# Optimization experiments

Hardware: AMD Instinct MI355X
Metric: run time of the kernel (lower is better)

Reference implementation:

```python
import jax, jax.numpy as jnp
import numpy as np

N_NODES = 50000
N_EDGES = 640000
N_GRAPHS = 64
IN_DIM, HID, OUT_DIM = 128, 256, 4


def gcn_conv(x, src, dst, W, b, n_nodes):
    """PyG GCNConv: linear transform, then sym-normalized aggregation with self-loops."""
    h = x @ W  # [N, out]
    deg = jnp.zeros((n_nodes,), h.dtype).at[dst].add(1.0) + 1.0  # +1 self-loop
    dinv = jax.lax.rsqrt(deg)  # deg >= 1 always
    norm = dinv[src] * dinv[dst]  # [E]
    msg = h[src] * norm[:, None]  # [E, out]  gather + scale
    agg = jax.ops.segment_sum(msg, dst, num_segments=n_nodes)  # scatter-add
    agg = agg + h * (dinv * dinv)[:, None]  # self-loop contribution
    return agg + b


def global_mean_pool(x, batch, num_graphs):
    s = jax.ops.segment_sum(x, batch, num_segments=num_graphs)
    cnt = jax.ops.segment_sum(jnp.ones((x.shape[0],), x.dtype), batch, num_segments=num_graphs)
    return s / jnp.clip(cnt, 1.0)[:, None]


def setup_inputs() -> dict:
    key = jax.random.key(0)
    ks = jax.random.split(key, 8)
    x = jax.random.normal(ks[0], (N_NODES, IN_DIM), jnp.float32)
    src = jax.random.randint(ks[1], (N_EDGES,), 0, N_NODES, jnp.int64 if jax.config.jax_enable_x64 else jnp.int32)
    dst = jax.random.randint(ks[2], (N_EDGES,), 0, N_NODES, src.dtype)
    batch = jnp.sort(jax.random.randint(ks[3], (N_NODES,), 0, N_GRAPHS, src.dtype))
    W1 = jax.random.normal(ks[4], (IN_DIM, HID), jnp.float32) * (1.0 / np.sqrt(IN_DIM))
    b1 = jnp.zeros((HID,), jnp.float32)
    W2 = jax.random.normal(ks[5], (HID, HID // 2), jnp.float32) * (1.0 / np.sqrt(HID))
    b2 = jnp.zeros((HID // 2,), jnp.float32)
    Wfc = jax.random.normal(ks[6], (HID // 2, OUT_DIM), jnp.float32) * (1.0 / np.sqrt(HID // 2))
    bfc = jnp.zeros((OUT_DIM,), jnp.float32)
    return {"x": x, "src": src, "dst": dst, "batch": batch,
            "W1": W1, "b1": b1, "W2": W2, "b2": b2, "Wfc": Wfc, "bfc": bfc}


def reference(x, src, dst, batch, W1, b1, W2, b2, Wfc, bfc):
    n = x.shape[0]
    h = jax.nn.relu(gcn_conv(x, src, dst, W1, b1, n))   # dropout is identity at inference
    h = jax.nn.relu(gcn_conv(h, src, dst, W2, b2, n))
    g = global_mean_pool(h, batch, N_GRAPHS)            # [G, HID//2]
    return g @ Wfc + bfc                                # [G, OUT_DIM]
```

## Files before the change

### kernel.cpp

```cpp
#include <hip/hip_runtime.h>


constexpr int IN_DIM  = 128;
constexpr int HID     = 256;
constexpr int HID2    = 128;
constexpr int OUT_DIM = 4;
constexpr int NGRAPH  = 64;
constexpr int TP      = 132;

typedef __attribute__((ext_vector_type(8))) short bf16x8;
typedef __attribute__((ext_vector_type(4))) float f32x4;

__device__ __forceinline__ short f2bf(float f) {
    union { float f; unsigned u; } v; v.f = f;
    unsigned r = v.u + 0x7fff + ((v.u >> 16) & 1);
    return (short)(r >> 16);
}
__device__ __forceinline__ float bf2f(short s) {
    union { unsigned u; float f; } v; v.u = ((unsigned)(unsigned short)s) << 16;
    return v.f;
}


__global__ void wprep_all_kernel(const float* __restrict__ W1, short* __restrict__ W1th,
                                 short* __restrict__ W1tl,
                                 const float* __restrict__ W2, short* __restrict__ W2th,
                                 short* __restrict__ W2tl,
                                 int* __restrict__ count, float* __restrict__ pool, int N) {
    int i = blockIdx.x * blockDim.x + threadIdx.x;
    if (i < IN_DIM * HID) {
        int k = i / HID, n = i % HID;
        float w = W1[i];
        short h = f2bf(w);
        W1th[n * IN_DIM + k] = h;
        W1tl[n * IN_DIM + k] = f2bf(w - bf2f(h));
    }
    if (i < HID * HID2) {
        int k = i / HID2, n = i % HID2;
        float w = W2[i];
        short h = f2bf(w);
        W2th[n * HID + k] = h;
        W2tl[n * HID + k] = f2bf(w - bf2f(h));
    }
    if (i < N) count[i] = 0;
    if (i < NGRAPH * HID2) pool[i] = 0.f;
}


__global__ void hist_kernel(const int* __restrict__ dst, int* __restrict__ count,
                            ushort* __restrict__ rank, int E) {
    int i = blockIdx.x * blockDim.x + threadIdx.x;
    if (i < E) rank[i] = (ushort)atomicAdd(&count[dst[i]], 1);
}

__global__ void scan1_kernel(const int* __restrict__ count, int* __restrict__ bsums, int N) {
    __shared__ int s[256];
    int t = threadIdx.x, i = blockIdx.x * 256 + t;
    int v = (i < N) ? count[i] : 0;
    s[t] = v; __syncthreads();
    for (int o = 1; o < 256; o <<= 1) {
        int x = (t >= o) ? s[t - o] : 0;
        __syncthreads(); s[t] += x; __syncthreads();
    }
    if (t == 255) bsums[blockIdx.x] = s[255];
}

__global__ void scan3_kernel(const int* __restrict__ count, const int* __restrict__ bsums,
                             int* __restrict__ rowptr, float* __restrict__ dinv,
                             int N, int E, int nb) {
    __shared__ int sb[256];
    __shared__ int s[256];
    int t = threadIdx.x, i = blockIdx.x * 256 + t;
    int bv = (t < nb) ? bsums[t] : 0;
    sb[t] = bv; __syncthreads();
    for (int o = 1; o < 256; o <<= 1) {
        int x = (t >= o) ? sb[t - o] : 0;
        __syncthreads(); sb[t] += x; __syncthreads();
    }
    int myex = (blockIdx.x == 0) ? 0 : sb[blockIdx.x - 1];
    int v = (i < N) ? count[i] : 0;
    s[t] = v; __syncthreads();
    for (int o = 1; o < 256; o <<= 1) {
        int x = (t >= o) ? s[t - o] : 0;
        __syncthreads(); s[t] += x; __syncthreads();
    }
    if (i < N) {
        rowptr[i] = myex + s[t] - v;
        dinv[i] = rsqrtf((float)v + 1.0f);
        if (i == 0) rowptr[N] = E;
    }
}

__global__ void scatter_scale_kernel(const int* __restrict__ src, const int* __restrict__ dst,
                                     const ushort* __restrict__ rank,
                                     const int* __restrict__ rowptr, ushort* __restrict__ csr,
                                     const float* __restrict__ x, const float* __restrict__ dinv,
                                     ushort* __restrict__ xb, int E, int total2) {
    int i = blockIdx.x * blockDim.x + threadIdx.x;
    if (i < E) {
        int p = rowptr[dst[i]] + (int)rank[i];
        csr[p] = (ushort)src[i];
    }
    if (i < total2) {
        float d = dinv[i >> 6];
        float2 v = ((const float2*)x)[i];
        ushort2 o;
        o.x = (ushort)f2bf(v.x * d);
        o.y = (ushort)f2bf(v.y * d);
        ((ushort2*)xb)[i] = o;
    }
}


template <int K, int N, bool ALO, bool RELU, bool SCALED>
__launch_bounds__(256)
__global__ void gemm_tile_kernel(const short* __restrict__ Ah, const short* __restrict__ Al,
                                 const short* __restrict__ Bh, const short* __restrict__ Bl,
                                 const float* __restrict__ bias,
                                 const float* __restrict__ dinv,
                                 short* __restrict__ Cb, int M) {
    __shared__ __align__(16) short LDSBUF[128 * TP];
    short (*S)[8][512] = (short (*)[8][512])LDSBUF;

    const int tid  = threadIdx.x;
    const int wave = tid >> 6;
    const int lane = tid & 63;
    const int row0 = blockIdx.y * 128;
    const int col0 = blockIdx.x * 128;

    const int l15 = lane & 15;
    const int kq  = (lane >> 4) * 8;

    f32x4 acc[4][4];
#pragma unroll
    for (int i = 0; i < 4; ++i)
#pragma unroll
        for (int j = 0; j < 4; ++j) acc[i][j] = f32x4{0.f, 0.f, 0.f, 0.f};

    const int mt0 = (wave & 1) * 4;
    const int nt0 = (wave >> 1) * 4;

    for (int kb = 0; kb < K; kb += 32) {
        if (ALO) {
            const short* gsrc = (wave == 0) ? Ah : (wave == 1) ? Al : (wave == 2) ? Bh : Bl;
            const bool isA = wave < 2;
            const int rb = (isA ? row0 : col0) + l15;
            bf16x8 stg[8];
#pragma unroll
            for (int j = 0; j < 8; ++j) {
                int rr = rb + j * 16;
                if (isA && rr >= M) rr = M - 1;
                stg[j] = *(const bf16x8*)(gsrc + (size_t)rr * K + kb + kq);
            }
#pragma unroll
            for (int j = 0; j < 8; ++j)
                *(bf16x8*)&S[wave][j][lane * 8] = stg[j];
        } else {
            if (wave < 2) {
                const int rb = row0 + l15;
                bf16x8 stg[4];
#pragma unroll
                for (int j = 0; j < 4; ++j) {
                    int rr = rb + (wave * 4 + j) * 16;
                    if (rr >= M) rr = M - 1;
                    stg[j] = *(const bf16x8*)(Ah + (size_t)rr * K + kb + kq);
                }
#pragma unroll
                for (int j = 0; j < 4; ++j)
                    *(bf16x8*)&S[0][wave * 4 + j][lane * 8] = stg[j];
            } else {
                const short* gsrc = (wave == 2) ? Bh : Bl;
                const int rb = col0 + l15;
                bf16x8 stg[8];
#pragma unroll
                for (int j = 0; j < 8; ++j)
                    stg[j] = *(const bf16x8*)(gsrc + (size_t)(rb + j * 16) * K + kb + kq);
#pragma unroll
                for (int j = 0; j < 8; ++j)
                    *(bf16x8*)&S[wave][j][lane * 8] = stg[j];
            }
        }
        __syncthreads();

        bf16x8 ah[4], al[4], bh[4], bl[4];
#pragma unroll
        for (int i = 0; i < 4; ++i) {
            ah[i] = *(const bf16x8*)&S[0][mt0 + i][lane * 8];
            if (ALO) al[i] = *(const bf16x8*)&S[1][mt0 + i][lane * 8];
            bh[i] = *(const bf16x8*)&S[2][nt0 + i][lane * 8];
            bl[i] = *(const bf16x8*)&S[3][nt0 + i][lane * 8];
        }
#pragma unroll
        for (int i = 0; i < 4; ++i)
#pragma unroll
            for (int j = 0; j < 4; ++j) {
                acc[i][j] = __builtin_amdgcn_mfma_f32_16x16x32_bf16(ah[i], bh[j], acc[i][j], 0, 0, 0);
                acc[i][j] = __builtin_amdgcn_mfma_f32_16x16x32_bf16(ah[i], bl[j], acc[i][j], 0, 0, 0);
                if (ALO)
                    acc[i][j] = __builtin_amdgcn_mfma_f32_16x16x32_bf16(al[i], bh[j], acc[i][j], 0, 0, 0);
            }
        __syncthreads();
    }

    short* T = LDSBUF;
    const int lrow_b = (wave & 1) * 64 + (lane >> 4) * 4;
    const int lcol_b = (wave >> 1) * 64 + l15;
#pragma unroll
    for (int j = 0; j < 4; ++j) {
        int lcol = lcol_b + j * 16;
        float bv = RELU ? bias[col0 + lcol] : 0.f;
#pragma unroll
        for (int i = 0; i < 4; ++i) {
#pragma unroll
            for (int r = 0; r < 4; ++r) {
                int lrow = lrow_b + i * 16 + r;
                float v = acc[i][j][r];
                if (RELU) v = fmaxf(v + bv, 0.f);
                if (SCALED) {
                    int dr = row0 + lrow; if (dr >= M) dr = M - 1;
                    v *= dinv[dr];
                }
                T[lrow * TP + lcol] = f2bf(v);
            }
        }
    }
    __syncthreads();
#pragma unroll
    for (int it = 0; it < 8; ++it) {
        int chunk = it * 256 + tid;
        int lr = chunk >> 4;
        int lc = (chunk & 15) * 8;
        int grow = row0 + lr;
        if (grow < M)
            *(bf16x8*)(Cb + (size_t)grow * N + col0 + lc) = *(const bf16x8*)&T[lr * TP + lc];
    }
}


template <bool POOL>
__launch_bounds__(256)
__global__ void agg_gather_kernel(const ushort* __restrict__ hb, const float* __restrict__ dinv,
                                  const int* __restrict__ rowptr, const ushort* __restrict__ csr,
                                  const float* __restrict__ bias,
                                  short* __restrict__ oh,
                                  const int* __restrict__ batch, float* __restrict__ pool,
                                  int N) {
    __shared__ float pacc[4][128];
    __shared__ int   sgid[4];

    const int tid  = threadIdx.x;
    const int wave = tid >> 6;
    const int lane = tid & 63;
    const int wid  = blockIdx.x * 4 + wave;
    const bool valid = wid < N;
    if (!POOL && !valid) return;
    const int cw = valid ? wid : N - 1;

    int lo = rowptr[cw], hi = rowptr[cw + 1];
    float dd = dinv[cw];

    const int g  = lane >> 4;
    const int li = lane & 15;

    float a[8];
    {
        bf16x8 sv = *(const bf16x8*)(hb + ((size_t)cw << 7) + (li << 3));
#pragma unroll
        for (int d = 0; d < 8; ++d) a[d] = (g == 0) ? bf2f(sv[d]) : 0.f;
    }

    const ushort* hrow = hb + (li << 3);

    for (int base = lo; base < hi; base += 64) {
        int cnt = min(64, hi - base);
        int sidx = (int)csr[base + (lane < cnt ? lane : cnt - 1)];
        int j = 0;
        for (; j + 32 <= cnt; j += 32) {
            bf16x8 p[8];
#pragma unroll
            for (int u = 0; u < 8; ++u) {
                int s = __shfl(sidx, j + u * 4 + g, 64);
                p[u] = *(const bf16x8*)(hrow + ((size_t)s << 7));
            }
#pragma unroll
            for (int u = 0; u < 8; ++u)
#pragma unroll
                for (int d = 0; d < 8; ++d) a[d] += bf2f(p[u][d]);
        }
        for (; j + 16 <= cnt; j += 16) {
            bf16x8 p[4];
#pragma unroll
            for (int u = 0; u < 4; ++u) {
                int s = __shfl(sidx, j + u * 4 + g, 64);
                p[u] = *(const bf16x8*)(hrow + ((size_t)s << 7));
            }
#pragma unroll
            for (int u = 0; u < 4; ++u)
#pragma unroll
                for (int d = 0; d < 8; ++d) a[d] += bf2f(p[u][d]);
        }
        if (j < cnt) {
            bf16x8 p[4];
            int e[4];
#pragma unroll
            for (int u = 0; u < 4; ++u) {
                e[u] = j + u * 4 + g;
                int s = __shfl(sidx, e[u] < cnt ? e[u] : cnt - 1, 64);
                p[u] = *(const bf16x8*)(hrow + ((size_t)s << 7));
            }
#pragma unroll
            for (int u = 0; u < 4; ++u) {
                bool v = e[u] < cnt;
#pragma unroll
                for (int d = 0; d < 8; ++d) a[d] += v ? bf2f(p[u][d]) : 0.f;
            }
        }
    }

#pragma unroll
    for (int d = 0; d < 8; ++d) {
        a[d] += __shfl_xor(a[d], 16, 64);
        a[d] += __shfl_xor(a[d], 32, 64);
        a[d] *= dd;
    }

    if (!POOL) {
        if (g == 0) {
            bf16x8 o;
#pragma unroll
            for (int d = 0; d < 8; ++d) o[d] = f2bf(a[d]);
            *(bf16x8*)&oh[(size_t)wid * 128 + li * 8] = o;
        }
        return;
    }

    {
        float4 b0 = ((const float4*)bias)[li * 2];
        float4 b1 = ((const float4*)bias)[li * 2 + 1];
        a[0] = fmaxf(a[0] + b0.x, 0.f); a[1] = fmaxf(a[1] + b0.y, 0.f);
        a[2] = fmaxf(a[2] + b0.z, 0.f); a[3] = fmaxf(a[3] + b0.w, 0.f);
        a[4] = fmaxf(a[4] + b1.x, 0.f); a[5] = fmaxf(a[5] + b1.y, 0.f);
        a[6] = fmaxf(a[6] + b1.z, 0.f); a[7] = fmaxf(a[7] + b1.w, 0.f);
    }
    if (lane == 0) sgid[wave] = valid ? batch[wid] : -1;
    if (g == 0) {
#pragma unroll
        for (int d = 0; d < 8; ++d) pacc[wave][li * 8 + d] = a[d];
    }
    __syncthreads();
    if (tid < 128) {
        int c = tid;
        int cur = sgid[0];
        float run = 0.f;
#pragma unroll
        for (int w = 0; w < 4; ++w) {
            int gi = sgid[w];
            if (gi < 0) break;
            if (gi != cur) { atomicAdd(&pool[cur * HID2 + c], run); run = 0.f; cur = gi; }
            run += pacc[w][c];
        }
        atomicAdd(&pool[cur * HID2 + c], run);
    }
}


__device__ __forceinline__ int lower_bound_i(const int* __restrict__ a, int n, int key) {
    int lo = 0, hi = n;
    while (lo < hi) {
        int mid = (lo + hi) >> 1;
        if (a[mid] < key) lo = mid + 1; else hi = mid;
    }
    return lo;
}

__global__ void fc_kernel(const float* __restrict__ pool, const int* __restrict__ batch,
                          const float* __restrict__ Wfc, const float* __restrict__ bfc,
                          float* __restrict__ out, int N) {
    int t = threadIdx.x;
    int g = t >> 2, o = t & 3;
    int lo = lower_bound_i(batch, N, g);
    int hi = lower_bound_i(batch, N, g + 1);
    float acc = 0.f;
#pragma unroll 8
    for (int c = 0; c < HID2; ++c)
        acc = fmaf(pool[g * HID2 + c], Wfc[c * OUT_DIM + o], acc);
    float inv = 1.0f / fmaxf((float)(hi - lo), 1.0f);
    out[g * OUT_DIM + o] = acc * inv + bfc[o];
}

extern "C" void kernel_launch(void* const* d_in, const int* in_sizes, int n_in,
                              void* d_out, int out_size, void* d_ws, size_t ws_size,
                              hipStream_t stream) {
    const float* x   = (const float*)d_in[0];
    const int* src   = (const int*)d_in[1];
    const int* dst   = (const int*)d_in[2];
    const int* batch = (const int*)d_in[3];
    const float* W1  = (const float*)d_in[4];
    const float* b1  = (const float*)d_in[5];
    const float* W2  = (const float*)d_in[6];
    const float* b2  = (const float*)d_in[7];
    const float* Wfc = (const float*)d_in[8];
    const float* bfc = (const float*)d_in[9];
    float* out = (float*)d_out;

    const int N = in_sizes[0] / IN_DIM;
    const int E = in_sizes[1];
    const int NB = (N + 255) / 256;

    char* ws = (char*)d_ws;
    size_t off = 0;
    auto alloc = [&](size_t bytes) {
        char* p = ws + off;
        off = (off + bytes + 255) & ~(size_t)255;
        return p;
    };
    float*  dinv   = (float*) alloc((size_t)N * 4);
    int*    count  = (int*)   alloc((size_t)N * 4);
    int*    rowptr = (int*)   alloc((size_t)(N + 1) * 4);
    int*    bsums  = (int*)   alloc(256 * 4);
    ushort* rank   = (ushort*)alloc((size_t)E * 2);
    ushort* csr    = (ushort*)alloc((size_t)E * 2);
    short*  W1th   = (short*) alloc((size_t)IN_DIM * HID * 2);
    short*  W1tl   = (short*) alloc((size_t)IN_DIM * HID * 2);
    short*  W2th   = (short*) alloc((size_t)HID * HID2 * 2);
    short*  W2tl   = (short*) alloc((size_t)HID * HID2 * 2);
    ushort* xb     = (ushort*)alloc((size_t)N * IN_DIM * 2);
    short*  axb    = (short*) alloc((size_t)N * IN_DIM * 2);
    short*  a1h    = (short*) alloc((size_t)N * HID * 2);
    float*  pool   = (float*) alloc((size_t)NGRAPH * HID2 * 4);
    ushort* h2b = xb;

    wprep_all_kernel<<<(max(IN_DIM * HID, N) + 255) / 256, 256, 0, stream>>>(
        W1, W1th, W1tl, W2, W2th, W2tl, count, pool, N);

    hist_kernel<<<(E + 255) / 256, 256, 0, stream>>>(dst, count, rank, E);
    scan1_kernel<<<NB, 256, 0, stream>>>(count, bsums, N);
    scan3_kernel<<<NB, 256, 0, stream>>>(count, bsums, rowptr, dinv, N, E, NB);
    scatter_scale_kernel<<<(N * 64 + 255) / 256, 256, 0, stream>>>(
        src, dst, rank, rowptr, csr, x, dinv, xb, E, N * 64);

    agg_gather_kernel<false><<<(N + 3) / 4, 256, 0, stream>>>(
        xb, dinv, rowptr, csr, nullptr, axb, nullptr, nullptr, N);
    gemm_tile_kernel<IN_DIM, HID, false, true, false>
        <<<dim3(HID / 128, (N + 127) / 128), 256, 0, stream>>>(
        axb, nullptr, W1th, W1tl, b1, nullptr, a1h, N);

    gemm_tile_kernel<HID, HID2, false, false, true>
        <<<dim3(HID2 / 128, (N + 127) / 128), 256, 0, stream>>>(
        a1h, nullptr, W2th, W2tl, nullptr, dinv, (short*)h2b, N);
    agg_gather_kernel<true><<<(N + 3) / 4, 256, 0, stream>>>(
        h2b, dinv, rowptr, csr, b2, nullptr, batch, pool, N);

    fc_kernel<<<1, NGRAPH * OUT_DIM, 0, stream>>>(pool, batch, Wfc, bfc, out, N);
}
```

Measured before the change: 249.0 us.

## Split neighbor aggregation into feature slices across blocks for gather cache locality

The gather-aggregation kernel now gives each block one 32-feature slice (64 bytes) of four nodes instead of the full 128-feature row. Block indices are interleaved so that the blocks covering one group of nodes, one per slice, run close together in time. Each lane group handles 16 edges per step over 4 sub-lanes, so every wave issues more independent edge loads, at the cost of 4x as many blocks and a wider shuffle reduction. Pool atomics are split per slice, and the pooling path skips blocks whose first node is out of range.

```diff
diff --git a/kernel.cpp b/kernel.cpp
--- a/kernel.cpp
+++ b/kernel.cpp
@@ -239,116 +239,109 @@
 
 template <bool POOL>
 __launch_bounds__(256)
-__global__ void agg_gather_kernel(const ushort* __restrict__ hb, const float* __restrict__ dinv,
-                                  const int* __restrict__ rowptr, const ushort* __restrict__ csr,
-                                  const float* __restrict__ bias,
-                                  short* __restrict__ oh,
-                                  const int* __restrict__ batch, float* __restrict__ pool,
-                                  int N) {
-    __shared__ float pacc[4][128];
+__global__ void agg_slice_kernel(const ushort* __restrict__ hb, const float* __restrict__ dinv,
+                                 const int* __restrict__ rowptr, const ushort* __restrict__ csr,
+                                 const float* __restrict__ bias,
+                                 short* __restrict__ oh,
+                                 const int* __restrict__ batch, float* __restrict__ pool,
+                                 int N) {
+    __shared__ float pacc[4][32];
     __shared__ int   sgid[4];
 
     const int tid  = threadIdx.x;
     const int wave = tid >> 6;
     const int lane = tid & 63;
-    const int wid  = blockIdx.x * 4 + wave;
-    const bool valid = wid < N;
+    const int bid  = blockIdx.x;
+    const int slice = (bid & 7) >> 1;
+    const int seq   = (bid >> 3) * 2 + (bid & 1);
+    const int node  = seq * 4 + wave;
+    const bool valid = node < N;
     if (!POOL && !valid) return;
-    const int cw = valid ? wid : N - 1;
-
-    int lo = rowptr[cw], hi = rowptr[cw + 1];
-    float dd = dinv[cw];
-
-    const int g  = lane >> 4;
-    const int li = lane & 15;
+    const int cw = valid ? node : N - 1;
+
+    const int lo = rowptr[cw], hi = rowptr[cw + 1];
+    const float dd = dinv[cw];
+
+    const int eg  = lane >> 2;
+    const int sub = lane & 3;
+    const int dbase = slice * 32 + sub * 8;
 
     float a[8];
     {
-        bf16x8 sv = *(const bf16x8*)(hb + ((size_t)cw << 7) + (li << 3));
-#pragma unroll
-        for (int d = 0; d < 8; ++d) a[d] = (g == 0) ? bf2f(sv[d]) : 0.f;
-    }
-
-    const ushort* hrow = hb + (li << 3);
+        bf16x8 sv = *(const bf16x8*)(hb + ((size_t)cw << 7) + dbase);
+#pragma unroll
+        for (int d = 0; d < 8; ++d) a[d] = (eg == 0) ? bf2f(sv[d]) : 0.f;
+    }
+
+    const ushort* hsl = hb + dbase;
 
     for (int base = lo; base < hi; base += 64) {
         int cnt = min(64, hi - base);
         int sidx = (int)csr[base + (lane < cnt ? lane : cnt - 1)];
         int j = 0;
         for (; j + 32 <= cnt; j += 32) {
-            bf16x8 p[8];
-#pragma unroll
-            for (int u = 0; u < 8; ++u) {
-                int s = __shfl(sidx, j + u * 4 + g, 64);
-                p[u] = *(const bf16x8*)(hrow + ((size_t)s << 7));
+            int s0 = __shfl(sidx, j + eg, 64);
+            int s1 = __shfl(sidx, j + 16 + eg, 64);
+            bf16x8 p0 = *(const bf16x8*)(hsl + ((size_t)s0 << 7));
+            bf16x8 p1 = *(const bf16x8*)(hsl + ((size_t)s1 << 7));
+#pragma unroll
+            for (int d = 0; d < 8; ++d) a[d] += bf2f(p0[d]);
+#pragma unroll
+            for (int d = 0; d < 8; ++d) a[d] += bf2f(p1[d]);
+        }
+        if (j < cnt) {
+            int rem = cnt - j;
+            int e0 = j + eg;
+            int s0 = __shfl(sidx, e0 < cnt ? e0 : cnt - 1, 64);
+            bf16x8 p0 = *(const bf16x8*)(hsl + ((size_t)s0 << 7));
+            if (rem > 16) {
+                int e1 = j + 16 + eg;
+                int s1 = __shfl(sidx, e1 < cnt ? e1 : cnt - 1, 64);
+                bf16x8 p1 = *(const bf16x8*)(hsl + ((size_t)s1 << 7));
+                bool v1 = e1 < cnt;
+#pragma unroll
+                for (int d = 0; d < 8; ++d) a[d] += v1 ? bf2f(p1[d]) : 0.f;
             }
-#pragma unroll
-            for (int u = 0; u < 8; ++u)
-#pragma unroll
-                for (int d = 0; d < 8; ++d) a[d] += bf2f(p[u][d]);
-        }
-        for (; j + 16 <= cnt; j += 16) {
-            bf16x8 p[4];
-#pragma unroll
-            for (int u = 0; u < 4; ++u) {
-                int s = __shfl(sidx, j + u * 4 + g, 64);
-                p[u] = *(const bf16x8*)(hrow + ((size_t)s << 7));
-            }
-#pragma unroll
-            for (int u = 0; u < 4; ++u)
-#pragma unroll
-                for (int d = 0; d < 8; ++d) a[d] += bf2f(p[u][d]);
-        }
-        if (j < cnt) {
-            bf16x8 p[4];
-            int e[4];
-#pragma unroll
-            for (int u = 0; u < 4; ++u) {
-                e[u] = j + u * 4 + g;
-                int s = __shfl(sidx, e[u] < cnt ? e[u] : cnt - 1, 64);
-                p[u] = *(const bf16x8*)(hrow + ((size_t)s << 7));
-            }
-#pragma unroll
-            for (int u = 0; u < 4; ++u) {
-                bool v = e[u] < cnt;
-#pragma unroll
-                for (int d = 0; d < 8; ++d) a[d] += v ? bf2f(p[u][d]) : 0.f;
-            }
+            bool v0 = e0 < cnt;
+#pragma unroll
+            for (int d = 0; d < 8; ++d) a[d] += v0 ? bf2f(p0[d]) : 0.f;
         }
     }
 
 #pragma unroll
     for (int d = 0; d < 8; ++d) {
+        a[d] += __shfl_xor(a[d], 4, 64);
+        a[d] += __shfl_xor(a[d], 8, 64);
         a[d] += __shfl_xor(a[d], 16, 64);
         a[d] += __shfl_xor(a[d], 32, 64);
         a[d] *= dd;
     }
 
     if (!POOL) {
-        if (g == 0) {
+        if (eg == 0) {
             bf16x8 o;
 #pragma unroll
             for (int d = 0; d < 8; ++d) o[d] = f2bf(a[d]);
-            *(bf16x8*)&oh[(size_t)wid * 128 + li * 8] = o;
+            *(bf16x8*)&oh[(size_t)node * 128 + dbase] = o;
         }
         return;
     }
 
     {
-        float4 b0 = ((const float4*)bias)[li * 2];
-        float4 b1 = ((const float4*)bias)[li * 2 + 1];
+        float4 b0 = ((const float4*)bias)[slice * 8 + sub * 2];
+        float4 b1 = ((const float4*)bias)[slice * 8 + sub * 2 + 1];
         a[0] = fmaxf(a[0] + b0.x, 0.f); a[1] = fmaxf(a[1] + b0.y, 0.f);
         a[2] = fmaxf(a[2] + b0.z, 0.f); a[3] = fmaxf(a[3] + b0.w, 0.f);
         a[4] = fmaxf(a[4] + b1.x, 0.f); a[5] = fmaxf(a[5] + b1.y, 0.f);
         a[6] = fmaxf(a[6] + b1.z, 0.f); a[7] = fmaxf(a[7] + b1.w, 0.f);
     }
-    if (lane == 0) sgid[wave] = valid ? batch[wid] : -1;
-    if (g == 0) {
-#pragma unroll
-        for (int d = 0; d < 8; ++d) pacc[wave][li * 8 + d] = a[d];
+    if (lane == 0) sgid[wave] = valid ? batch[node] : -1;
+    if (eg == 0) {
+#pragma unroll
+        for (int d = 0; d < 8; ++d) pacc[wave][sub * 8 + d] = a[d];
     }
     __syncthreads();
-    if (tid < 128) {
+    if (tid < 32 && sgid[0] >= 0) {
         int c = tid;
         int cur = sgid[0];
         float run = 0.f;
@@ -356,10 +349,10 @@
         for (int w = 0; w < 4; ++w) {
             int gi = sgid[w];
             if (gi < 0) break;
-            if (gi != cur) { atomicAdd(&pool[cur * HID2 + c], run); run = 0.f; cur = gi; }
+            if (gi != cur) { atomicAdd(&pool[cur * HID2 + slice * 32 + c], run); run = 0.f; cur = gi; }
             run += pacc[w][c];
         }
-        atomicAdd(&pool[cur * HID2 + c], run);
+        atomicAdd(&pool[cur * HID2 + slice * 32 + c], run);
     }
 }
 
@@ -406,6 +399,7 @@
     const int N = in_sizes[0] / IN_DIM;
     const int E = in_sizes[1];
     const int NB = (N + 255) / 256;
+    const int GA = ((N + 7) / 8) * 8;
 
     char* ws = (char*)d_ws;
     size_t off = 0;
@@ -439,7 +433,7 @@
     scatter_scale_kernel<<<(N * 64 + 255) / 256, 256, 0, stream>>>(
         src, dst, rank, rowptr, csr, x, dinv, xb, E, N * 64);
 
-    agg_gather_kernel<false><<<(N + 3) / 4, 256, 0, stream>>>(
+    agg_slice_kernel<false><<<GA, 256, 0, stream>>>(
         xb, dinv, rowptr, csr, nullptr, axb, nullptr, nullptr, N);
     gemm_tile_kernel<IN_DIM, HID, false, true, false>
         <<<dim3(HID / 128, (N + 127) / 128), 256, 0, stream>>>(
@@ -448,7 +442,7 @@
     gemm_tile_kernel<HID, HID2, false, false, true>
         <<<dim3(HID2 / 128, (N + 127) / 128), 256, 0, stream>>>(
         a1h, nullptr, W2th, W2tl, nullptr, dinv, (short*)h2b, N);
-    agg_gather_kernel<true><<<(N + 3) / 4, 256, 0, stream>>>(
+    agg_slice_kernel<true><<<GA, 256, 0, stream>>>(
         h2b, dinv, rowptr, csr, b2, nullptr, batch, pool, N);
 
     fc_kernel<<<1, NGRAPH * OUT_DIM, 0, stream>>>(pool, batch, Wfc, bfc, out, N);
```

Measured after the change: 346.0 us. +38.9%, slower.

## Aggregate one node per 16-lane group instead of one node per wavefront

Applied to the files above, without the earlier changes.

The CSR gather-aggregation kernel now gives each node to a 16-lane group, so four nodes share a wavefront and sixteen share a block, instead of one node per 64-lane wavefront with four sub-groups splitting its edges. Each group loads its neighbor indices in chunks of 16 and issues up to 16 row loads per chunk, which removes the cross-group shuffle reduction. With an average degree of about 13, the old layout left most of each wavefront's 64 edge slots empty; the new layout is meant to use those lanes. The cost is masked wasted loads when a node's degree is below 16, and more divergence inside a wavefront from uneven degrees. The pooling epilogue now walks 16 node slots per block.

```diff
diff --git a/kernel.cpp b/kernel.cpp
--- a/kernel.cpp
+++ b/kernel.cpp
@@ -239,97 +239,72 @@
 
 template <bool POOL>
 __launch_bounds__(256)
-__global__ void agg_gather_kernel(const ushort* __restrict__ hb, const float* __restrict__ dinv,
-                                  const int* __restrict__ rowptr, const ushort* __restrict__ csr,
-                                  const float* __restrict__ bias,
-                                  short* __restrict__ oh,
-                                  const int* __restrict__ batch, float* __restrict__ pool,
-                                  int N) {
-    __shared__ float pacc[4][128];
-    __shared__ int   sgid[4];
+__global__ void agg_group_kernel(const ushort* __restrict__ hb, const float* __restrict__ dinv,
+                                 const int* __restrict__ rowptr, const ushort* __restrict__ csr,
+                                 const float* __restrict__ bias,
+                                 short* __restrict__ oh,
+                                 const int* __restrict__ batch, float* __restrict__ pool,
+                                 int N) {
+    __shared__ float pacc[16][128];
+    __shared__ int   sgid[16];
 
     const int tid  = threadIdx.x;
-    const int wave = tid >> 6;
-    const int lane = tid & 63;
-    const int wid  = blockIdx.x * 4 + wave;
-    const bool valid = wid < N;
-    if (!POOL && !valid) return;
-    const int cw = valid ? wid : N - 1;
-
-    int lo = rowptr[cw], hi = rowptr[cw + 1];
-    float dd = dinv[cw];
-
-    const int g  = lane >> 4;
-    const int li = lane & 15;
+    const int li   = tid & 15;
+    const int nib  = tid >> 4;
+    const int node = blockIdx.x * 16 + nib;
+    const bool valid = node < N;
+    const int cw = valid ? node : N - 1;
+
+    const int lo = rowptr[cw], hi = rowptr[cw + 1];
+    const float dd = dinv[cw];
 
     float a[8];
     {
         bf16x8 sv = *(const bf16x8*)(hb + ((size_t)cw << 7) + (li << 3));
 #pragma unroll
-        for (int d = 0; d < 8; ++d) a[d] = (g == 0) ? bf2f(sv[d]) : 0.f;
-    }
-
-    const ushort* hrow = hb + (li << 3);
-
-    for (int base = lo; base < hi; base += 64) {
-        int cnt = min(64, hi - base);
-        int sidx = (int)csr[base + (lane < cnt ? lane : cnt - 1)];
-        int j = 0;
-        for (; j + 32 <= cnt; j += 32) {
-            bf16x8 p[8];
-#pragma unroll
-            for (int u = 0; u < 8; ++u) {
-                int s = __shfl(sidx, j + u * 4 + g, 64);
-                p[u] = *(const bf16x8*)(hrow + ((size_t)s << 7));
-            }
-#pragma unroll
-            for (int u = 0; u < 8; ++u)
-#pragma unroll
-                for (int d = 0; d < 8; ++d) a[d] += bf2f(p[u][d]);
-        }
-        for (; j + 16 <= cnt; j += 16) {
-            bf16x8 p[4];
-#pragma unroll
-            for (int u = 0; u < 4; ++u) {
-                int s = __shfl(sidx, j + u * 4 + g, 64);
-                p[u] = *(const bf16x8*)(hrow + ((size_t)s << 7));
-            }
-#pragma unroll
-            for (int u = 0; u < 4; ++u)
-#pragma unroll
-                for (int d = 0; d < 8; ++d) a[d] += bf2f(p[u][d]);
-        }
-        if (j < cnt) {
-            bf16x8 p[4];
-            int e[4];
-#pragma unroll
-            for (int u = 0; u < 4; ++u) {
-                e[u] = j + u * 4 + g;
-                int s = __shfl(sidx, e[u] < cnt ? e[u] : cnt - 1, 64);
-                p[u] = *(const bf16x8*)(hrow + ((size_t)s << 7));
-            }
-#pragma unroll
-            for (int u = 0; u < 4; ++u) {
-                bool v = e[u] < cnt;
-#pragma unroll
-                for (int d = 0; d < 8; ++d) a[d] += v ? bf2f(p[u][d]) : 0.f;
-            }
-        }
-    }
-
-#pragma unroll
-    for (int d = 0; d < 8; ++d) {
-        a[d] += __shfl_xor(a[d], 16, 64);
-        a[d] += __shfl_xor(a[d], 32, 64);
-        a[d] *= dd;
-    }
+        for (int d = 0; d < 8; ++d) a[d] = bf2f(sv[d]);
+    }
+
+    const ushort* hsl = hb + (li << 3);
+
+    for (int base = lo; base < hi; base += 16) {
+        int cnt = min(16, hi - base);
+        int sidx = (int)csr[base + (li < cnt ? li : cnt - 1)];
+        bf16x8 p[8], q[8];
+#pragma unroll
+        for (int u = 0; u < 8; ++u) {
+            int s = __shfl(sidx, u < cnt ? u : cnt - 1, 16);
+            p[u] = *(const bf16x8*)(hsl + ((size_t)s << 7));
+        }
+#pragma unroll
+        for (int u = 0; u < 8; ++u) {
+            int e = 8 + u;
+            int s = __shfl(sidx, e < cnt ? e : cnt - 1, 16);
+            q[u] = *(const bf16x8*)(hsl + ((size_t)s << 7));
+        }
+#pragma unroll
+        for (int u = 0; u < 8; ++u) {
+            bool v = u < cnt;
+#pragma unroll
+            for (int d = 0; d < 8; ++d) a[d] += v ? bf2f(p[u][d]) : 0.f;
+        }
+#pragma unroll
+        for (int u = 0; u < 8; ++u) {
+            bool v = 8 + u < cnt;
+#pragma unroll
+            for (int d = 0; d < 8; ++d) a[d] += v ? bf2f(q[u][d]) : 0.f;
+        }
+    }
+
+#pragma unroll
+    for (int d = 0; d < 8; ++d) a[d] *= dd;
 
     if (!POOL) {
-        if (g == 0) {
+        if (valid) {
             bf16x8 o;
 #pragma unroll
             for (int d = 0; d < 8; ++d) o[d] = f2bf(a[d]);
-            *(bf16x8*)&oh[(size_t)wid * 128 + li * 8] = o;
+            *(bf16x8*)&oh[(size_t)node * 128 + li * 8] = o;
         }
         return;
     }
@@ -342,18 +317,16 @@
         a[4] = fmaxf(a[4] + b1.x, 0.f); a[5] = fmaxf(a[5] + b1.y, 0.f);
         a[6] = fmaxf(a[6] + b1.z, 0.f); a[7] = fmaxf(a[7] + b1.w, 0.f);
     }
-    if (lane == 0) sgid[wave] = valid ? batch[wid] : -1;
-    if (g == 0) {
-#pragma unroll
-        for (int d = 0; d < 8; ++d) pacc[wave][li * 8 + d] = a[d];
-    }
+    if (li == 0) sgid[nib] = valid ? batch[node] : -1;
+#pragma unroll
+    for (int d = 0; d < 8; ++d) pacc[nib][li * 8 + d] = a[d];
     __syncthreads();
     if (tid < 128) {
         int c = tid;
         int cur = sgid[0];
         float run = 0.f;
-#pragma unroll
-        for (int w = 0; w < 4; ++w) {
+#pragma unroll 1
+        for (int w = 0; w < 16; ++w) {
             int gi = sgid[w];
             if (gi < 0) break;
             if (gi != cur) { atomicAdd(&pool[cur * HID2 + c], run); run = 0.f; cur = gi; }
@@ -406,6 +379,7 @@
     const int N = in_sizes[0] / IN_DIM;
     const int E = in_sizes[1];
     const int NB = (N + 255) / 256;
+    const int GA = (N + 15) / 16;
 
     char* ws = (char*)d_ws;
     size_t off = 0;
@@ -439,7 +413,7 @@
     scatter_scale_kernel<<<(N * 64 + 255) / 256, 256, 0, stream>>>(
         src, dst, rank, rowptr, csr, x, dinv, xb, E, N * 64);
 
-    agg_gather_kernel<false><<<(N + 3) / 4, 256, 0, stream>>>(
+    agg_group_kernel<false><<<GA, 256, 0, stream>>>(
         xb, dinv, rowptr, csr, nullptr, axb, nullptr, nullptr, N);
     gemm_tile_kernel<IN_DIM, HID, false, true, false>
         <<<dim3(HID / 128, (N + 127) / 128), 256, 0, stream>>>(
@@ -448,7 +422,7 @@
     gemm_tile_kernel<HID, HID2, false, false, true>
         <<<dim3(HID2 / 128, (N + 127) / 128), 256, 0, stream>>>(
         a1h, nullptr, W2th, W2tl, nullptr, dinv, (short*)h2b, N);
-    agg_gather_kernel<true><<<(N + 3) / 4, 256, 0, stream>>>(
+    agg_group_kernel<true><<<GA, 256, 0, stream>>>(
         h2b, dinv, rowptr, csr, b2, nullptr, batch, pool, N);
 
     fc_kernel<<<1, NGRAPH * OUT_DIM, 0, stream>>>(pool, batch, Wfc, bfc, out, N);
```

Result: faster. 242.7 us (-2.5%).
